# Kernel tuning notes

Measured on AMD Instinct MI355X. Metric: run time of the kernel, lower is better.

The kernel has to match this reference:

```python
import jax, jax.numpy as jnp
import numpy as np

B, T, SD = 16, 512, 64          # batch, action seq len, sample_dim
EMB, HD = 1024, 64              # emb_dim, head_dim
NH = EMB // HD                  # 16 heads
DEPTH, NREG, LAT, FF = 8, 16, 256, 4 * EMB
S = T + NREG                    # total sequence length (actions + registers)


def setup_inputs() -> dict:
    key = jax.random.key(0)
    ks = jax.random.split(key, 16)
    def n(k, shape, scale=0.02):
        return jax.random.normal(k, shape, jnp.float32) * scale
    return {
        "sample": jax.random.normal(ks[0], (B, T, SD), jnp.float32),
        "W_emb": n(ks[1], (SD, EMB)), "b_emb": jnp.zeros((EMB,), jnp.float32),
        "pos": n(ks[2], (T, EMB)),
        "registers": n(ks[3], (NREG, EMB), 1.0),
        "ln1_s": jnp.ones((DEPTH, EMB), jnp.float32), "ln1_b": jnp.zeros((DEPTH, EMB), jnp.float32),
        "W_qkv": n(ks[4], (DEPTH, EMB, 3 * EMB)), "b_qkv": jnp.zeros((DEPTH, 3 * EMB), jnp.float32),
        "W_o": n(ks[5], (DEPTH, EMB, EMB)), "b_o": jnp.zeros((DEPTH, EMB), jnp.float32),
        "ln2_s": jnp.ones((DEPTH, EMB), jnp.float32), "ln2_b": jnp.zeros((DEPTH, EMB), jnp.float32),
        "W_fc1": n(ks[6], (DEPTH, EMB, FF)), "b_fc1": jnp.zeros((DEPTH, FF), jnp.float32),
        "W_fc2": n(ks[7], (DEPTH, FF, EMB)), "b_fc2": jnp.zeros((DEPTH, EMB), jnp.float32),
        "lnf_s": jnp.ones((EMB,), jnp.float32), "lnf_b": jnp.zeros((EMB,), jnp.float32),
        "W_head": n(ks[8], (EMB, LAT)), "b_head": jnp.zeros((LAT,), jnp.float32),
    }


def _ln(x, s, b):
    m = jnp.mean(x, -1, keepdims=True)
    v = jnp.var(x, -1, keepdims=True)
    return (x - m) * jax.lax.rsqrt(v + 1e-5) * s + b


def _causal_last_mask():
    # True = attended to. Actions attend to all actions but NOT registers;
    # registers attend to all actions and causally (incl. self) to registers.
    allowed = jnp.ones((S, S), jnp.bool_)
    allowed = allowed.at[:T, T:].set(False)
    allowed = allowed.at[T:, T:].set(jnp.tril(jnp.ones((NREG, NREG), jnp.bool_)))
    return allowed


def reference(sample, W_emb, b_emb, pos, registers, ln1_s, ln1_b, W_qkv, b_qkv,
              W_o, b_o, ln2_s, ln2_b, W_fc1, b_fc1, W_fc2, b_fc2,
              lnf_s, lnf_b, W_head, b_head):
    # embed + positional add
    x = sample @ W_emb + b_emb + pos[None, :, :]          # [B,T,E]
    # concat registers
    x = jnp.concatenate([x, jnp.broadcast_to(registers, (B, NREG, EMB))], axis=1)  # [B,S,E]
    mask = _causal_last_mask()                             # [S,S]
    scale = 1.0 / jnp.sqrt(jnp.asarray(HD, x.dtype))
    for i in range(DEPTH):
        # pre-LN multi-head attention with structured block mask
        h = _ln(x, ln1_s[i], ln1_b[i])
        qkv = h @ W_qkv[i] + b_qkv[i]
        q, k, v = jnp.split(qkv, 3, axis=-1)
        q = q.reshape(B, S, NH, HD)
        k = k.reshape(B, S, NH, HD)
        v = v.reshape(B, S, NH, HD)
        att = jnp.einsum('bqhd,bkhd->bhqk', q, k) * scale
        att = jnp.where(mask[None, None], att, jnp.finfo(att.dtype).min)
        att = jax.nn.softmax(att, axis=-1)
        o = jnp.einsum('bhqk,bkhd->bqhd', att, v).reshape(B, S, EMB)
        x = x + o @ W_o[i] + b_o[i]
        # pre-LN MLP
        h2 = _ln(x, ln2_s[i], ln2_b[i])
        x = x + jax.nn.gelu(h2 @ W_fc1[i] + b_fc1[i]) @ W_fc2[i] + b_fc2[i]
    x = _ln(x, lnf_s, lnf_b)
    # head applied to register positions only
    return x[:, T:] @ W_head + b_head                      # [B,NREG,LAT]
```

## Files before the change

kernel.cpp:

```cpp
#include <hip/hip_runtime.h>
#include <hip/hip_bf16.h>


typedef unsigned short u16;
typedef __attribute__((ext_vector_type(4))) float f32x4;
typedef __attribute__((ext_vector_type(8))) __bf16 bf16x8;

#define DEV static __device__ __forceinline__

constexpr int Bb = 16, Tt = 512, E = 1024, HD = 64, NHd = 16;
constexpr int DEPTH = 8, NREG = 16, LAT = 256, FF = 4096;
constexpr int S = Tt + NREG;
constexpr int SPAD = 576;
constexpr int MR = Bb * S;
constexpr int ME = Bb * Tt;

DEV u16 f2bf(float f) {
  unsigned u = __builtin_bit_cast(unsigned, f);
  u += 0x7fffu + ((u >> 16) & 1u);
  return (u16)(u >> 16);
}

DEV void gll16(const u16* g, u16* l) {
  __builtin_amdgcn_global_load_lds((const __attribute__((address_space(1))) void*)g,
                                   (__attribute__((address_space(3))) void*)l, 16, 0, 0);
}

enum { M_EMBED, M_QKV, M_OPROJ, M_FC1, M_FC2, M_HEAD };

struct GA {
  const u16* A; const u16* Bt;
  int K, lda, ldb, Nrows, ldc;
  const float* bias; const float* pos;
  float* fout; u16* bout;
  u16 *qp, *kp, *vtp;
};

template<int MODE, int BN>
__global__ __launch_bounds__(256)
void gemm_bt(GA g) {
  constexpr int NI = BN / 32;
  __shared__ __align__(16) u16 As[2][128 * 32];
  __shared__ __align__(16) u16 Bs[2][BN * 32];
  const int tid = threadIdx.x;
  const u16* A  = g.A;
  const u16* Bt = g.Bt;

  int tM, tN;
  {
    const int nwg = gridDim.x * gridDim.y;
    int flat = blockIdx.y * gridDim.x + blockIdx.x;
    const int q = nwg >> 3, r = nwg & 7;
    const int xcd = flat & 7, loc = flat >> 3;
    flat = (xcd < r ? xcd * (q + 1) : r * (q + 1) + (xcd - r) * q) + loc;
    tM = flat / gridDim.x; tN = flat % gridDim.x;
  }

  const int lane = tid & 63, wid = tid >> 6;
  const int wr = wid >> 1, wc = wid & 1;
  const int fr = lane & 15, fg = lane >> 4;

  const int arow = tM * 128 + (tid >> 2);
  int br0 = tN * BN + (tid >> 2);
  if (br0 > g.Nrows - 1) br0 = g.Nrows - 1;
  int br1 = tN * BN + 64 + (tid >> 2);
  if (br1 > g.Nrows - 1) br1 = g.Nrows - 1;
  const int kseg = (tid & 3) * 8;
  const int woff = (tid & 192) * 8;

  const u16* ag0 = A  + (long)arow        * g.lda + kseg;
  const u16* ag1 = A  + (long)(arow + 64) * g.lda + kseg;
  const u16* bg0 = Bt + (long)br0         * g.ldb + kseg;
  const u16* bg1 = Bt + (long)br1         * g.ldb + kseg;

  f32x4 acc[4][NI];
#pragma unroll
  for (int i = 0; i < 4; ++i)
#pragma unroll
    for (int j = 0; j < NI; ++j) acc[i][j] = f32x4{0.f, 0.f, 0.f, 0.f};

  const int nk = g.K >> 5;
  {
    gll16(ag0, &As[0][woff]);
    gll16(ag1, &As[0][woff + 2048]);
    gll16(bg0, &Bs[0][woff]);
    if (BN == 128) gll16(bg1, &Bs[0][woff + 2048]);
  }
  __syncthreads();

  for (int kt = 0; kt < nk; ++kt) {
    const int cur = kt & 1;
    if (kt + 1 < nk) {
      const int k0 = (kt + 1) << 5;
      gll16(ag0 + k0, &As[cur ^ 1][woff]);
      gll16(ag1 + k0, &As[cur ^ 1][woff + 2048]);
      gll16(bg0 + k0, &Bs[cur ^ 1][woff]);
      if (BN == 128) gll16(bg1 + k0, &Bs[cur ^ 1][woff + 2048]);
    }
    bf16x8 af[4], bfr[NI];
#pragma unroll
    for (int mi = 0; mi < 4; ++mi)
      af[mi] = *(const bf16x8*)&As[cur][(wr * 64 + mi * 16 + fr) * 32 + fg * 8];
#pragma unroll
    for (int ni = 0; ni < NI; ++ni)
      bfr[ni] = *(const bf16x8*)&Bs[cur][(wc * (BN / 2) + ni * 16 + fr) * 32 + fg * 8];
#pragma unroll
    for (int mi = 0; mi < 4; ++mi)
#pragma unroll
      for (int ni = 0; ni < NI; ++ni)
        acc[mi][ni] = __builtin_amdgcn_mfma_f32_16x16x32_bf16(af[mi], bfr[ni], acc[mi][ni], 0, 0, 0);
    __syncthreads();
  }

#pragma unroll
  for (int mi = 0; mi < 4; ++mi)
#pragma unroll
    for (int ni = 0; ni < NI; ++ni)
#pragma unroll
      for (int j = 0; j < 4; ++j) {
        const int row = tM * 128 + wr * 64 + mi * 16 + fg * 4 + j;
        const int col = tN * BN + wc * (BN / 2) + ni * 16 + fr;
        float v = acc[mi][ni][j];
        if (MODE == M_EMBED) {
          const int b = row >> 9, t = row & 511;
          v += g.bias[col] + g.pos[(long)t * E + col];
          g.fout[((long)(b * S + t)) * E + col] = v;
        } else if (MODE == M_QKV) {
          const int b = row / S, s = row - b * S;
          v += g.bias[col];
          const int part = col >> 10, c = col & 1023;
          const int hh = c >> 6, d = c & 63;
          const u16 bf = f2bf(v);
          if (part == 0)      g.qp [((long)((b * NHd + hh) * SPAD + s)) * HD + d] = bf;
          else if (part == 1) g.kp [((long)((b * NHd + hh) * SPAD + s)) * HD + d] = bf;
          else                g.vtp[((long)((b * NHd + hh) * HD   + d)) * SPAD + s] = bf;
        } else if (MODE == M_OPROJ || MODE == M_FC2) {
          const long idx = (long)row * g.ldc + col;
          g.fout[idx] += v + g.bias[col];
        } else if (MODE == M_FC1) {
          v += g.bias[col];
          const float z = 0.7978845608028654f * (v + 0.044715f * v * v * v);
          const float e = __expf(2.f * z);
          const float th = 1.f - 2.f / (e + 1.f);
          g.bout[(long)row * g.ldc + col] = f2bf(0.5f * v * (1.f + th));
        } else if (MODE == M_HEAD) {
          g.fout[(long)row * g.ldc + col] = v + g.bias[col];
        }
      }
}

__global__ __launch_bounds__(256)
void flash_k(const u16* __restrict__ q, const u16* __restrict__ k,
             const u16* __restrict__ vt, u16* __restrict__ o) {
  __shared__ __align__(16) u16 Ks[64 * 64];
  __shared__ __align__(16) u16 Vs[64 * 64];
  __shared__ __align__(16) u16 Ps[4 * 16 * 64];
  const int tid = threadIdx.x;
  const int lane = tid & 63, w = tid >> 6;
  const int fr = lane & 15, fg = lane >> 4;

  int flat = blockIdx.y * 9 + blockIdx.x;
  flat = (flat & 7) * 288 + (flat >> 3);
  const int bh = flat / 9, qt = flat % 9;
  const int q0 = qt * 64;

  const u16* qrow = q + ((long)bh * SPAD + q0 + w * 16 + fr) * HD;
  const bf16x8 qf0 = *(const bf16x8*)(qrow + fg * 8);
  const bf16x8 qf1 = *(const bf16x8*)(qrow + 32 + fg * 8);

  const int srow = lane >> 3, sseg = (lane & 7) * 8;
  const u16* kg = k  + ((long)bh * SPAD + w * 16 + srow) * HD + sseg;
  const u16* vg = vt + ((long)(bh * HD + w * 16 + srow)) * SPAD + sseg;
  u16* lk = Ks + w * 16 * HD;
  u16* lv = Vs + w * 16 * HD;

  float m[4], lsum[4]; f32x4 oa[4];
#pragma unroll
  for (int j = 0; j < 4; ++j) { m[j] = -1e30f; lsum[j] = 0.f; }
#pragma unroll
  for (int n = 0; n < 4; ++n) oa[n] = f32x4{0.f, 0.f, 0.f, 0.f};

  const int nt = (q0 < Tt) ? 8 : 9;
  for (int kt = 0; kt < nt; ++kt) {
    __syncthreads();
    gll16(kg + kt * 64 * HD,          lk);
    gll16(kg + kt * 64 * HD + 8 * HD, lk + 8 * HD);
    gll16(vg + kt * 64,               lv);
    gll16(vg + kt * 64 + 8 * SPAD,    lv + 8 * HD);
    __syncthreads();

    f32x4 sfr[4];
#pragma unroll
    for (int n = 0; n < 4; ++n) {
      const bf16x8 kf0 = *(const bf16x8*)&Ks[(n * 16 + fr) * HD + fg * 8];
      const bf16x8 kf1 = *(const bf16x8*)&Ks[(n * 16 + fr) * HD + 32 + fg * 8];
      sfr[n] = __builtin_amdgcn_mfma_f32_16x16x32_bf16(qf0, kf0, f32x4{0.f,0.f,0.f,0.f}, 0, 0, 0);
      sfr[n] = __builtin_amdgcn_mfma_f32_16x16x32_bf16(qf1, kf1, sfr[n], 0, 0, 0);
    }
    float p[4][4];
#pragma unroll
    for (int j = 0; j < 4; ++j) {
      const int qg = q0 + w * 16 + fg * 4 + j;
      const int vlim = qg < Tt ? Tt : qg + 1;
#pragma unroll
      for (int n = 0; n < 4; ++n) {
        const int col = kt * 64 + n * 16 + fr;
        p[n][j] = (col < vlim) ? sfr[n][j] * 0.125f : -1e30f;
      }
    }
#pragma unroll
    for (int j = 0; j < 4; ++j) {
      float pm = fmaxf(fmaxf(p[0][j], p[1][j]), fmaxf(p[2][j], p[3][j]));
#pragma unroll
      for (int msk = 1; msk <= 8; msk <<= 1) pm = fmaxf(pm, __shfl_xor(pm, msk));
      const float mn = fmaxf(m[j], pm);
      const float corr = __expf(m[j] - mn);
      m[j] = mn;
      float rs = 0.f;
#pragma unroll
      for (int n = 0; n < 4; ++n) { const float e = __expf(p[n][j] - mn); p[n][j] = e; rs += e; }
#pragma unroll
      for (int msk = 1; msk <= 8; msk <<= 1) rs += __shfl_xor(rs, msk);
      lsum[j] = lsum[j] * corr + rs;
#pragma unroll
      for (int n = 0; n < 4; ++n) oa[n][j] *= corr;
    }
#pragma unroll
    for (int j = 0; j < 4; ++j)
#pragma unroll
      for (int n = 0; n < 4; ++n)
        Ps[w * 1024 + (fg * 4 + j) * 64 + n * 16 + fr] = f2bf(p[n][j]);
    __syncthreads();
    const bf16x8 pf0 = *(const bf16x8*)&Ps[w * 1024 + fr * 64 + fg * 8];
    const bf16x8 pf1 = *(const bf16x8*)&Ps[w * 1024 + fr * 64 + 32 + fg * 8];
#pragma unroll
    for (int n = 0; n < 4; ++n) {
      const bf16x8 vf0 = *(const bf16x8*)&Vs[(n * 16 + fr) * HD + fg * 8];
      const bf16x8 vf1 = *(const bf16x8*)&Vs[(n * 16 + fr) * HD + 32 + fg * 8];
      oa[n] = __builtin_amdgcn_mfma_f32_16x16x32_bf16(pf0, vf0, oa[n], 0, 0, 0);
      oa[n] = __builtin_amdgcn_mfma_f32_16x16x32_bf16(pf1, vf1, oa[n], 0, 0, 0);
    }
  }

  const int b = bh >> 4, hh = bh & 15;
#pragma unroll
  for (int j = 0; j < 4; ++j) {
    const int qg = q0 + w * 16 + fg * 4 + j;
    if (qg < S) {
      const float inv = 1.f / lsum[j];
#pragma unroll
      for (int n = 0; n < 4; ++n)
        o[((long)(b * S + qg)) * E + hh * HD + n * 16 + fr] = f2bf(oa[n][j] * inv);
    }
  }
}

__global__ __launch_bounds__(256)
void ln_k(const float* __restrict__ x, const float* __restrict__ sc,
          const float* __restrict__ bi, u16* __restrict__ out, int gather) {
  const int r = blockIdx.x;
  const int srow = gather ? ((r >> 4) * S + Tt + (r & 15)) : r;
  const float4 v = ((const float4*)(x + (long)srow * E))[threadIdx.x];
  float s = v.x + v.y + v.z + v.w;
  float q = v.x * v.x + v.y * v.y + v.z * v.z + v.w * v.w;
#pragma unroll
  for (int o = 32; o; o >>= 1) { s += __shfl_down(s, o); q += __shfl_down(q, o); }
  __shared__ float ps[8];
  if ((threadIdx.x & 63) == 0) { ps[threadIdx.x >> 6] = s; ps[4 + (threadIdx.x >> 6)] = q; }
  __syncthreads();
  s = ps[0] + ps[1] + ps[2] + ps[3];
  q = ps[4] + ps[5] + ps[6] + ps[7];
  const float mean = s * (1.f / E);
  const float rs = rsqrtf(q * (1.f / E) - mean * mean + 1e-5f);
  const int c = threadIdx.x * 4;
  ushort4 o4;
  o4.x = f2bf((v.x - mean) * rs * sc[c + 0] + bi[c + 0]);
  o4.y = f2bf((v.y - mean) * rs * sc[c + 1] + bi[c + 1]);
  o4.z = f2bf((v.z - mean) * rs * sc[c + 2] + bi[c + 2]);
  o4.w = f2bf((v.w - mean) * rs * sc[c + 3] + bi[c + 3]);
  ((ushort4*)(out + (long)r * E))[threadIdx.x] = o4;
}

__global__ __launch_bounds__(256)
void wtrans(const float* __restrict__ src, u16* __restrict__ dst, int R, int C) {
  __shared__ float t[32][33];
  const int c0 = blockIdx.x * 32, r0 = blockIdx.y * 32;
  const int tx = threadIdx.x & 31, ty = threadIdx.x >> 5;
#pragma unroll
  for (int i = 0; i < 32; i += 8) t[ty + i][tx] = src[(long)(r0 + ty + i) * C + c0 + tx];
  __syncthreads();
#pragma unroll
  for (int i = 0; i < 32; i += 8) dst[(long)(c0 + ty + i) * R + r0 + tx] = f2bf(t[tx][ty + i]);
}

__global__ void cvt_bf(const float* __restrict__ in, u16* __restrict__ out, long n) {
  const long i = ((long)blockIdx.x * blockDim.x + threadIdx.x) * 4;
  if (i >= n) return;
  const float4 v = *(const float4*)(in + i);
  ushort4 o; o.x = f2bf(v.x); o.y = f2bf(v.y); o.z = f2bf(v.z); o.w = f2bf(v.w);
  *(ushort4*)(out + i) = o;
}

__global__ void zero_k(float4* p, long n) {
  long i = (long)blockIdx.x * blockDim.x + threadIdx.x;
  const long st = (long)gridDim.x * blockDim.x;
  const float4 z = make_float4(0.f, 0.f, 0.f, 0.f);
  for (; i < n; i += st) p[i] = z;
}

__global__ void reg_copy(const float* __restrict__ regs, float* __restrict__ x) {
  const int b = blockIdx.x >> 4, r = blockIdx.x & 15;
  const float4* sp = (const float4*)(regs + (long)r * E);
  float4* dp = (float4*)(x + ((long)(b * S + Tt + r)) * E);
  dp[threadIdx.x] = sp[threadIdx.x];
}

constexpr long OFF_WQKV = 0L;
constexpr long OFF_WO   = OFF_WQKV + 3072L * 1024 * 2;
constexpr long OFF_WFC1 = OFF_WO   + 1024L * 1024 * 2;
constexpr long OFF_WFC2 = OFF_WFC1 + 4096L * 1024 * 2;
constexpr long OFF_WEMB = OFF_WFC2 + 1024L * 4096 * 2;
constexpr long OFF_WHEAD= OFF_WEMB + 1024L * 64 * 2;
constexpr long OFF_SMP  = OFF_WHEAD+ 256L * 1024 * 2;
constexpr long OFF_X    = OFF_SMP  + (long)ME * 64 * 2;
constexpr long OFF_H    = OFF_X    + (long)MR * E * 4;
constexpr long OFF_Q    = OFF_H    + (long)MR * E * 2;
constexpr long OFF_K    = OFF_Q    + 256L * SPAD * HD * 2;
constexpr long OFF_VT   = OFF_K    + 256L * SPAD * HD * 2;
constexpr long OFF_O    = OFF_VT   + 256L * SPAD * HD * 2;
constexpr long OFF_HF   = OFF_O    + (long)MR * FF * 2;
constexpr long WS_NEED  = OFF_HF   + 256L * 1024 * 2;

extern "C" void kernel_launch(void* const* d_in, const int* in_sizes, int n_in,
                              void* d_out, int out_size, void* d_ws, size_t ws_size,
                              hipStream_t stream) {
  if (ws_size < (size_t)WS_NEED) return;

  const float* sample = (const float*)d_in[0];
  const float* W_emb  = (const float*)d_in[1];
  const float* b_emb  = (const float*)d_in[2];
  const float* pos    = (const float*)d_in[3];
  const float* regs   = (const float*)d_in[4];
  const float* ln1_s  = (const float*)d_in[5];
  const float* ln1_b  = (const float*)d_in[6];
  const float* W_qkv  = (const float*)d_in[7];
  const float* b_qkv  = (const float*)d_in[8];
  const float* W_o    = (const float*)d_in[9];
  const float* b_o    = (const float*)d_in[10];
  const float* ln2_s  = (const float*)d_in[11];
  const float* ln2_b  = (const float*)d_in[12];
  const float* W_fc1  = (const float*)d_in[13];
  const float* b_fc1  = (const float*)d_in[14];
  const float* W_fc2  = (const float*)d_in[15];
  const float* b_fc2  = (const float*)d_in[16];
  const float* lnf_s  = (const float*)d_in[17];
  const float* lnf_b  = (const float*)d_in[18];
  const float* W_head = (const float*)d_in[19];
  const float* b_head = (const float*)d_in[20];

  char* w = (char*)d_ws;
  u16* wqkvT = (u16*)(w + OFF_WQKV);
  u16* woT   = (u16*)(w + OFF_WO);
  u16* wfc1T = (u16*)(w + OFF_WFC1);
  u16* wfc2T = (u16*)(w + OFF_WFC2);
  u16* wembT = (u16*)(w + OFF_WEMB);
  u16* wheadT= (u16*)(w + OFF_WHEAD);
  u16* smp   = (u16*)(w + OFF_SMP);
  float* x   = (float*)(w + OFF_X);
  u16* h     = (u16*)(w + OFF_H);
  u16* qp    = (u16*)(w + OFF_Q);
  u16* kp    = (u16*)(w + OFF_K);
  u16* vtp   = (u16*)(w + OFF_VT);
  u16* o     = (u16*)(w + OFF_O);
  u16* a1    = (u16*)(w + OFF_O);
  u16* hf    = (u16*)(w + OFF_HF);

  wtrans<<<dim3(32, 2, 1), 256, 0, stream>>>(W_emb,  wembT, 64, 1024);
  wtrans<<<dim3(8, 32, 1), 256, 0, stream>>>(W_head, wheadT, 1024, 256);
  cvt_bf<<<dim3(512), 256, 0, stream>>>(sample, smp, (long)ME * 64);
  zero_k<<<dim3(2048), 256, 0, stream>>>((float4*)qp, (3L * 256 * SPAD * HD * 2) / 16);

  {
    GA g{}; g.A = smp; g.Bt = wembT; g.K = 64; g.lda = 64; g.ldb = 64;
    g.Nrows = E; g.bias = b_emb; g.pos = pos; g.fout = x;
    gemm_bt<M_EMBED, 64><<<dim3(16, 64, 1), 256, 0, stream>>>(g);
  }
  reg_copy<<<dim3(256), 256, 0, stream>>>(regs, x);

  for (int L = 0; L < DEPTH; ++L) {
    wtrans<<<dim3(96, 32, 1),  256, 0, stream>>>(W_qkv + (long)L * 1024 * 3072, wqkvT, 1024, 3072);
    wtrans<<<dim3(32, 32, 1),  256, 0, stream>>>(W_o   + (long)L * 1024 * 1024, woT,   1024, 1024);
    wtrans<<<dim3(128, 32, 1), 256, 0, stream>>>(W_fc1 + (long)L * 1024 * 4096, wfc1T, 1024, 4096);
    wtrans<<<dim3(32, 128, 1), 256, 0, stream>>>(W_fc2 + (long)L * 4096 * 1024, wfc2T, 4096, 1024);

    ln_k<<<dim3(MR), 256, 0, stream>>>(x, ln1_s + L * E, ln1_b + L * E, h, 0);
    {
      GA g{}; g.A = h; g.Bt = wqkvT;
      g.K = 1024; g.lda = 1024; g.ldb = 1024; g.Nrows = 3072;
      g.bias = b_qkv + L * 3072; g.qp = qp; g.kp = kp; g.vtp = vtp;
      gemm_bt<M_QKV, 128><<<dim3(24, 66, 1), 256, 0, stream>>>(g);
    }
    flash_k<<<dim3(9, 256, 1), 256, 0, stream>>>(qp, kp, vtp, o);
    {
      GA g{}; g.A = o; g.Bt = woT;
      g.K = 1024; g.lda = 1024; g.ldb = 1024; g.Nrows = 1024; g.ldc = 1024;
      g.bias = b_o + L * E; g.fout = x;
      gemm_bt<M_OPROJ, 128><<<dim3(8, 66, 1), 256, 0, stream>>>(g);
    }
    ln_k<<<dim3(MR), 256, 0, stream>>>(x, ln2_s + L * E, ln2_b + L * E, h, 0);
    {
      GA g{}; g.A = h; g.Bt = wfc1T;
      g.K = 1024; g.lda = 1024; g.ldb = 1024; g.Nrows = 4096; g.ldc = 4096;
      g.bias = b_fc1 + L * FF; g.bout = a1;
      gemm_bt<M_FC1, 128><<<dim3(32, 66, 1), 256, 0, stream>>>(g);
    }
    {
      GA g{}; g.A = a1; g.Bt = wfc2T;
      g.K = 4096; g.lda = 4096; g.ldb = 4096; g.Nrows = 1024; g.ldc = 1024;
      g.bias = b_fc2 + L * E; g.fout = x;
      gemm_bt<M_FC2, 128><<<dim3(8, 66, 1), 256, 0, stream>>>(g);
    }
  }

  ln_k<<<dim3(256), 256, 0, stream>>>(x, lnf_s, lnf_b, hf, 1);
  {
    GA g{}; g.A = hf; g.Bt = wheadT; g.K = 1024; g.lda = 1024; g.ldb = 1024;
    g.Nrows = LAT; g.ldc = LAT; g.bias = b_head; g.fout = (float*)d_out;
    gemm_bt<M_HEAD, 128><<<dim3(2, 2, 1), 256, 0, stream>>>(g);
  }
}
```

Baseline: 3.948 ms.

## Triple-buffer GEMM LDS with vmcnt waits, XOR swizzle, and MFMA priority

Moves the GEMM mainloop from double to triple buffering with global-to-LDS loads issued two tiles ahead. Each iteration waits on vmcnt and a single barrier instead of syncing at both ends. An XOR swizzle on the K-segment placement removes LDS bank conflicts on fragment reads, and setprio raises wave priority around the MFMA block. This costs more LDS per block, which may lower occupancy, and it relies on exact vmcnt counts for correctness.

New measurement: 3.895 ms. No clear change (-1.3%).

```diff
diff --git a/kernel.cpp b/kernel.cpp
--- a/kernel.cpp
+++ b/kernel.cpp
@@ -40,8 +40,8 @@
 __global__ __launch_bounds__(256)
 void gemm_bt(GA g) {
   constexpr int NI = BN / 32;
-  __shared__ __align__(16) u16 As[2][128 * 32];
-  __shared__ __align__(16) u16 Bs[2][BN * 32];
+  __shared__ __align__(16) u16 As[3][128 * 32];
+  __shared__ __align__(16) u16 Bs[3][BN * 32];
   const int tid = threadIdx.x;
   const u16* A  = g.A;
   const u16* Bt = g.Bt;
@@ -65,7 +65,7 @@
   if (br0 > g.Nrows - 1) br0 = g.Nrows - 1;
   int br1 = tN * BN + 64 + (tid >> 2);
   if (br1 > g.Nrows - 1) br1 = g.Nrows - 1;
-  const int kseg = (tid & 3) * 8;
+  const int kseg = ((tid & 3) ^ ((tid >> 3) & 3)) * 8;
   const int woff = (tid & 192) * 8;
 
   const u16* ag0 = A  + (long)arow        * g.lda + kseg;
@@ -79,38 +79,49 @@
 #pragma unroll
     for (int j = 0; j < NI; ++j) acc[i][j] = f32x4{0.f, 0.f, 0.f, 0.f};
 
+#define STAGE(KT, BUF) do {                                   \
+    const int _k0 = (KT) << 5;                                \
+    gll16(ag0 + _k0, &As[BUF][woff]);                         \
+    gll16(ag1 + _k0, &As[BUF][woff + 2048]);                  \
+    gll16(bg0 + _k0, &Bs[BUF][woff]);                         \
+    if (BN == 128) gll16(bg1 + _k0, &Bs[BUF][woff + 2048]);   \
+  } while (0)
+
   const int nk = g.K >> 5;
-  {
-    gll16(ag0, &As[0][woff]);
-    gll16(ag1, &As[0][woff + 2048]);
-    gll16(bg0, &Bs[0][woff]);
-    if (BN == 128) gll16(bg1, &Bs[0][woff + 2048]);
-  }
-  __syncthreads();
+  STAGE(0, 0);
+  if (nk > 1) STAGE(1, 1);
+
+  const int rsw = (fg ^ ((fr >> 1) & 3)) * 8;
 
   for (int kt = 0; kt < nk; ++kt) {
-    const int cur = kt & 1;
-    if (kt + 1 < nk) {
-      const int k0 = (kt + 1) << 5;
-      gll16(ag0 + k0, &As[cur ^ 1][woff]);
-      gll16(ag1 + k0, &As[cur ^ 1][woff + 2048]);
-      gll16(bg0 + k0, &Bs[cur ^ 1][woff]);
-      if (BN == 128) gll16(bg1 + k0, &Bs[cur ^ 1][woff + 2048]);
-    }
+    const int cur = kt % 3;
+    if (kt < nk - 1) {
+      if constexpr (BN == 128) asm volatile("s_waitcnt vmcnt(4)" ::: "memory");
+      else                     asm volatile("s_waitcnt vmcnt(3)" ::: "memory");
+    } else {
+      asm volatile("s_waitcnt vmcnt(0)" ::: "memory");
+    }
+    __builtin_amdgcn_sched_barrier(0);
+    __builtin_amdgcn_s_barrier();
+    __builtin_amdgcn_sched_barrier(0);
+    if (kt + 2 < nk) STAGE(kt + 2, (kt + 2) % 3);
+
     bf16x8 af[4], bfr[NI];
 #pragma unroll
     for (int mi = 0; mi < 4; ++mi)
-      af[mi] = *(const bf16x8*)&As[cur][(wr * 64 + mi * 16 + fr) * 32 + fg * 8];
+      af[mi] = *(const bf16x8*)&As[cur][(wr * 64 + mi * 16 + fr) * 32 + rsw];
 #pragma unroll
     for (int ni = 0; ni < NI; ++ni)
-      bfr[ni] = *(const bf16x8*)&Bs[cur][(wc * (BN / 2) + ni * 16 + fr) * 32 + fg * 8];
+      bfr[ni] = *(const bf16x8*)&Bs[cur][(wc * (BN / 2) + ni * 16 + fr) * 32 + rsw];
+    __builtin_amdgcn_s_setprio(1);
 #pragma unroll
     for (int mi = 0; mi < 4; ++mi)
 #pragma unroll
       for (int ni = 0; ni < NI; ++ni)
         acc[mi][ni] = __builtin_amdgcn_mfma_f32_16x16x32_bf16(af[mi], bfr[ni], acc[mi][ni], 0, 0, 0);
-    __syncthreads();
-  }
+    __builtin_amdgcn_s_setprio(0);
+  }
+#undef STAGE
 
 #pragma unroll
   for (int mi = 0; mi < 4; ++mi)
```
